# Kernel optimization log

Hardware: AMD Instinct MI355X
Metric: run time of the kernel (lower is better)

## Reference

```python
import jax, jax.numpy as jnp
import numpy as np

NUM_EXPERTS = 8
TOP_K = 2

def setup_inputs() -> dict:
    key = jax.random.key(0)
    k1, k2, k3, k4 = jax.random.split(key, 4)
    B, T, C, F = 4, 2048, 1024, 4096
    x = jax.random.normal(k1, (B, T, C), dtype=jnp.float32)
    gate_w = jax.random.normal(k2, (C, NUM_EXPERTS), dtype=jnp.float32) * 0.02
    w1 = jax.random.normal(k3, (NUM_EXPERTS, C, F), dtype=jnp.float32) * 0.02
    w2 = jax.random.normal(k4, (NUM_EXPERTS, F, C), dtype=jnp.float32) * 0.02
    return {"x": x, "gate_w": gate_w, "w1": w1, "w2": w2}

def reference(x, gate_w, w1, w2):
    # Router: softmax over experts, then top-k and renormalize
    router_logits = jnp.einsum('btc,ce->bte', x, gate_w)          # [B,T,E]
    routing = jax.nn.softmax(router_logits, axis=-1)
    topw, topi = jax.lax.top_k(routing, TOP_K)                    # [B,T,K]
    topw = topw / jnp.sum(topw, axis=-1, keepdims=True)
    # Combined per-expert weight per token (zero if not selected)
    onehot = jax.nn.one_hot(topi, NUM_EXPERTS, dtype=x.dtype)     # [B,T,K,E]
    combine = jnp.einsum('btk,btke->bte', topw, onehot)           # [B,T,E]
    # Expert FFNs (exact GELU, matching torch nn.GELU default)
    out = jnp.zeros_like(x)
    for e in range(NUM_EXPERTS):
        h = jax.nn.gelu(jnp.einsum('btc,cf->btf', x, w1[e]), approximate=False)
        y = jnp.einsum('btf,fc->btc', h, w2[e])
        out = out + combine[..., e:e+1] * y
    return out
```

## Files before the change

### kernel.cpp

```cpp
#include <hip/hip_runtime.h>
#include <hip/hip_bf16.h>
#include <math.h>

#define NUM_EXPERTS 8
#define NTOK 8192
#define CDIM 1024
#define FDIM 4096
#define MAXSLOTS 17408
#define MAXTILES 136
#define TILES_PER_XCD 17

typedef __bf16 bf16x8 __attribute__((ext_vector_type(8)));
typedef float  f32x4  __attribute__((ext_vector_type(4)));

#define GPTR(p) ((const __attribute__((address_space(1))) unsigned int*)(p))
#define LPTR(p) ((__attribute__((address_space(3))) unsigned int*)(p))

__device__ __forceinline__ float gelu_exact(float v){
  return 0.5f * v * (1.0f + erff(v * 0.70710678118654752f));
}
__device__ __forceinline__ float bf2f(unsigned short u){
  union { unsigned int i; float f; } cv; cv.i = ((unsigned int)u) << 16; return cv.f;
}

__global__ __launch_bounds__(256) void moe_router(
    const float* __restrict__ x, const float* __restrict__ gw,
    int2* __restrict__ topi, float2* __restrict__ topw, int* __restrict__ counts)
{
  int token = blockIdx.x * 4 + (threadIdx.x >> 6);
  int lane  = threadIdx.x & 63;
  int e = lane & 7, part = lane >> 3;
  const float* xr = x + (size_t)token * CDIM;
  float s = 0.f;
  int c0 = part * 128;
  for (int c = c0; c < c0 + 128; ++c) s += xr[c] * gw[c * 8 + e];
  s += __shfl_xor(s, 8); s += __shfl_xor(s, 16); s += __shfl_xor(s, 32);
  float m1 = s; int i1 = e;
  for (int off = 1; off < 8; off <<= 1){
    float ov = __shfl_xor(m1, off); int oi = __shfl_xor(i1, off);
    if (ov > m1 || (ov == m1 && oi < i1)){ m1 = ov; i1 = oi; }
  }
  float l2 = (e == i1) ? -INFINITY : s;
  float m2 = l2; int i2 = e;
  for (int off = 1; off < 8; off <<= 1){
    float ov = __shfl_xor(m2, off); int oi = __shfl_xor(i2, off);
    if (ov > m2 || (ov == m2 && oi < i2)){ m2 = ov; i2 = oi; }
  }
  if (lane == 0){
    float r = expf(m2 - m1);
    float wa = 1.f / (1.f + r);
    topi[token] = make_int2(i1, i2);
    topw[token] = make_float2(wa, 1.f - wa);
    atomicAdd(&counts[i1], 1);
    atomicAdd(&counts[i2], 1);
  }
}

__global__ __launch_bounds__(256) void convert_x_kernel(
    const float* __restrict__ x, __hip_bfloat16* __restrict__ xb)
{
  int i = (blockIdx.x * 256 + threadIdx.x) * 4;
  float4 v = *(const float4*)(x + i);
  union { __hip_bfloat16 hh[4]; ushort4 u; } cv;
  cv.hh[0] = __float2bfloat16(v.x);
  cv.hh[1] = __float2bfloat16(v.y);
  cv.hh[2] = __float2bfloat16(v.z);
  cv.hh[3] = __float2bfloat16(v.w);
  *(ushort4*)(xb + i) = cv.u;
}

__global__ __launch_bounds__(256) void transpose_bf16_kernel(
    const float* __restrict__ in, __hip_bfloat16* __restrict__ outp, int R, int Cc)
{
  __shared__ __hip_bfloat16 tile[64 * 66];
  const size_t msz = (size_t)R * Cc;
  const float* inm = in + (size_t)blockIdx.z * msz;
  __hip_bfloat16* outm = outp + (size_t)blockIdx.z * msz;
  int r0 = blockIdx.y * 64, c0 = blockIdx.x * 64;
  int t = threadIdx.x;
  int r = t & 63, cseg = (t >> 6) * 16;
  const float* src = inm + (size_t)(r0 + r) * Cc + c0 + cseg;
  float4 v0 = ((const float4*)src)[0];
  float4 v1 = ((const float4*)src)[1];
  float4 v2 = ((const float4*)src)[2];
  float4 v3 = ((const float4*)src)[3];
  float vv[16] = {v0.x,v0.y,v0.z,v0.w, v1.x,v1.y,v1.z,v1.w,
                  v2.x,v2.y,v2.z,v2.w, v3.x,v3.y,v3.z,v3.w};
#pragma unroll
  for (int k = 0; k < 16; ++k)
    tile[(cseg + k) * 66 + r] = __float2bfloat16(vv[k]);
  __syncthreads();
#pragma unroll
  for (int p = 0; p < 2; ++p){
    int cc = p * 32 + (t >> 3), ch = (t & 7) * 8;
    const unsigned short* rowp = (const unsigned short*)tile + cc * 66 + ch;
    unsigned int a = *(const unsigned int*)(rowp + 0);
    unsigned int b = *(const unsigned int*)(rowp + 2);
    unsigned int c = *(const unsigned int*)(rowp + 4);
    unsigned int d = *(const unsigned int*)(rowp + 6);
    *(uint4*)(outm + (size_t)(c0 + cc) * R + r0 + ch) = make_uint4(a, b, c, d);
  }
}

__global__ void scan_kernel(const int* __restrict__ counts, int* cursors, int* num_tiles,
    int* tile_expert, int* tile_slotbase, int* slot_token, float* slot_weight)
{
  int t = threadIdx.x;
  if (t == 0){
    int base = 0, T = 0;
    for (int e = 0; e < NUM_EXPERTS; ++e){
      cursors[e] = base;
      int nt = (counts[e] + 127) >> 7;
      for (int i = 0; i < nt; ++i){ tile_expert[T] = e; tile_slotbase[T] = base + i * 128; ++T; }
      base += nt << 7;
    }
    *num_tiles = T;
  }
  for (int i = t; i < MAXSLOTS; i += 256){ slot_token[i] = 0; slot_weight[i] = 0.f; }
}

__global__ void assign_kernel(const int2* __restrict__ topi, const float2* __restrict__ topw,
    int* cursors, int* slot_token, float* slot_weight, int2* __restrict__ token_slots)
{
  int token = blockIdx.x * 256 + threadIdx.x;
  int2 ii = topi[token];
  float2 ww = topw[token];
  int p0 = atomicAdd(&cursors[ii.x], 1);
  slot_token[p0] = token; slot_weight[p0] = ww.x;
  int p1 = atomicAdd(&cursors[ii.y], 1);
  slot_token[p1] = token; slot_weight[p1] = ww.y;
  token_slots[token] = make_int2(p0, p1);
}

template<int KD, int ND, bool G1>
__global__ __launch_bounds__(512, 4) void moe_gemm(
    const __hip_bfloat16* __restrict__ A, const __hip_bfloat16* __restrict__ Bw,
    __hip_bfloat16* __restrict__ Out,
    const int* __restrict__ num_tiles, const int* __restrict__ tile_expert,
    const int* __restrict__ tile_slotbase, const int* __restrict__ slot_token)
{
  constexpr int NT = KD / 32;
  constexpr int NBLK = ND / 256;
  __shared__ __align__(16) char smem[73728];
  const int L = blockIdx.x;
  const int xcd = L & 7;
  const int jdec = L >> 3;
  const int tl = jdec / NBLK;
  const int nb = jdec % NBLK;
  const int tm = xcd * TILES_PER_XCD + tl;
  if (tm >= *num_tiles) return;
  const int e = tile_expert[tm];
  const int sbase = tile_slotbase[tm];
  const int n0 = nb * 256;
  const int t = threadIdx.x;
  const int lane = t & 63, wid = t >> 6;
  const int wm = wid >> 2, wn = wid & 3;
  const int lr = lane & 15, lq = lane >> 4;

  const int arowi = sbase + wid * 16 + lr;
  const int arow = G1 ? slot_token[arowi] : arowi;
  const __hip_bfloat16* srcA  = A  + (size_t)arow * KD + lq * 8;
  const __hip_bfloat16* srcB0 = Bw + ((size_t)e * ND + n0 + wid * 16 + lr) * KD + lq * 8;
  const __hip_bfloat16* srcB1 = srcB0 + (size_t)128 * KD;
  char* dA  = smem + wid * 1024;
  char* dB0 = smem + 24576 + wid * 1024;
  char* dB1 = dB0 + 8192;

#define STG_A(kt, ss) __builtin_amdgcn_global_load_lds(GPTR(srcA + (size_t)(kt) * 32), LPTR(dA + (ss) * 8192), 16, 0, 0)
#define STG_B(kt, ss) do{ \
    __builtin_amdgcn_global_load_lds(GPTR(srcB0 + (size_t)(kt) * 32), LPTR(dB0 + (ss) * 16384), 16, 0, 0); \
    __builtin_amdgcn_global_load_lds(GPTR(srcB1 + (size_t)(kt) * 32), LPTR(dB1 + (ss) * 16384), 16, 0, 0); }while(0)

  STG_A(0, 0); STG_B(0, 0);
  STG_A(1, 1); STG_B(1, 1);

  f32x4 acc[4][4] = {};
  const char* rdA = smem + (wm * 4) * 1024 + lane * 16;
  const char* rdB = smem + 24576 + (wn * 4) * 1024 + lane * 16;

  asm volatile("s_waitcnt vmcnt(3)\n\ts_barrier" ::: "memory");
  __builtin_amdgcn_sched_barrier(0);

  int s = 0;
  for (int kt = 0; kt < NT; ++kt){
    int s2 = s + 2; if (s2 >= 3) s2 -= 3;
    const char* pA = rdA + s * 8192;
    const char* pB = rdB + s * 16384;
    bf16x8 b0 = *(const bf16x8*)(pB);
    bf16x8 b1 = *(const bf16x8*)(pB + 1024);
    bf16x8 b2 = *(const bf16x8*)(pB + 2048);
    bf16x8 b3 = *(const bf16x8*)(pB + 3072);
    bf16x8 a0 = *(const bf16x8*)(pA);
    bf16x8 a1 = *(const bf16x8*)(pA + 1024);
    if (kt + 2 < NT) STG_A(kt + 2, s2);
    __builtin_amdgcn_s_setprio(1);
    acc[0][0] = __builtin_amdgcn_mfma_f32_16x16x32_bf16(b0, a0, acc[0][0], 0, 0, 0);
    acc[0][1] = __builtin_amdgcn_mfma_f32_16x16x32_bf16(b1, a0, acc[0][1], 0, 0, 0);
    acc[0][2] = __builtin_amdgcn_mfma_f32_16x16x32_bf16(b2, a0, acc[0][2], 0, 0, 0);
    acc[0][3] = __builtin_amdgcn_mfma_f32_16x16x32_bf16(b3, a0, acc[0][3], 0, 0, 0);
    acc[1][0] = __builtin_amdgcn_mfma_f32_16x16x32_bf16(b0, a1, acc[1][0], 0, 0, 0);
    acc[1][1] = __builtin_amdgcn_mfma_f32_16x16x32_bf16(b1, a1, acc[1][1], 0, 0, 0);
    acc[1][2] = __builtin_amdgcn_mfma_f32_16x16x32_bf16(b2, a1, acc[1][2], 0, 0, 0);
    acc[1][3] = __builtin_amdgcn_mfma_f32_16x16x32_bf16(b3, a1, acc[1][3], 0, 0, 0);
    __builtin_amdgcn_s_setprio(0);
    a0 = *(const bf16x8*)(pA + 2048);
    a1 = *(const bf16x8*)(pA + 3072);
    if (kt + 2 < NT) STG_B(kt + 2, s2);
    __builtin_amdgcn_s_setprio(1);
    acc[2][0] = __builtin_amdgcn_mfma_f32_16x16x32_bf16(b0, a0, acc[2][0], 0, 0, 0);
    acc[2][1] = __builtin_amdgcn_mfma_f32_16x16x32_bf16(b1, a0, acc[2][1], 0, 0, 0);
    acc[2][2] = __builtin_amdgcn_mfma_f32_16x16x32_bf16(b2, a0, acc[2][2], 0, 0, 0);
    acc[2][3] = __builtin_amdgcn_mfma_f32_16x16x32_bf16(b3, a0, acc[2][3], 0, 0, 0);
    acc[3][0] = __builtin_amdgcn_mfma_f32_16x16x32_bf16(b0, a1, acc[3][0], 0, 0, 0);
    acc[3][1] = __builtin_amdgcn_mfma_f32_16x16x32_bf16(b1, a1, acc[3][1], 0, 0, 0);
    acc[3][2] = __builtin_amdgcn_mfma_f32_16x16x32_bf16(b2, a1, acc[3][2], 0, 0, 0);
    acc[3][3] = __builtin_amdgcn_mfma_f32_16x16x32_bf16(b3, a1, acc[3][3], 0, 0, 0);
    __builtin_amdgcn_s_setprio(0);
    if (kt < NT - 2){
      asm volatile("s_waitcnt vmcnt(3)\n\ts_barrier" ::: "memory");
      __builtin_amdgcn_sched_barrier(0);
    } else if (kt < NT - 1){
      asm volatile("s_waitcnt vmcnt(0)\n\ts_barrier" ::: "memory");
      __builtin_amdgcn_sched_barrier(0);
    }
    s = (s == 2) ? 0 : s + 1;
  }
#undef STG_A
#undef STG_B

  const int orow0 = sbase + wm * 64 + lr;
  const int ocol0 = n0 + wn * 64 + lq * 4;
#pragma unroll
  for (int i = 0; i < 4; ++i){
    __hip_bfloat16* orow = Out + (size_t)(orow0 + i * 16) * ND + ocol0;
#pragma unroll
    for (int j2 = 0; j2 < 4; ++j2){
      f32x4 v = acc[i][j2];
      union { __hip_bfloat16 h4[4]; ushort4 u; } cv;
      if (G1){
        cv.h4[0] = __float2bfloat16(gelu_exact(v[0]));
        cv.h4[1] = __float2bfloat16(gelu_exact(v[1]));
        cv.h4[2] = __float2bfloat16(gelu_exact(v[2]));
        cv.h4[3] = __float2bfloat16(gelu_exact(v[3]));
      } else {
        cv.h4[0] = __float2bfloat16(v[0]);
        cv.h4[1] = __float2bfloat16(v[1]);
        cv.h4[2] = __float2bfloat16(v[2]);
        cv.h4[3] = __float2bfloat16(v[3]);
      }
      *(ushort4*)(orow + j2 * 16) = cv.u;
    }
  }
}

__global__ __launch_bounds__(256) void combine_kernel(
    const __hip_bfloat16* __restrict__ y, const int2* __restrict__ token_slots,
    const float* __restrict__ slot_weight, float* __restrict__ out)
{
  int token = blockIdx.x;
  int c = threadIdx.x * 4;
  int2 ss = token_slots[token];
  float w0 = slot_weight[ss.x], w1 = slot_weight[ss.y];
  ushort4 a = *(const ushort4*)((const unsigned short*)y + (size_t)ss.x * CDIM + c);
  ushort4 b = *(const ushort4*)((const unsigned short*)y + (size_t)ss.y * CDIM + c);
  float4 o;
  o.x = w0 * bf2f(a.x) + w1 * bf2f(b.x);
  o.y = w0 * bf2f(a.y) + w1 * bf2f(b.y);
  o.z = w0 * bf2f(a.z) + w1 * bf2f(b.z);
  o.w = w0 * bf2f(a.w) + w1 * bf2f(b.w);
  *(float4*)(out + (size_t)token * CDIM + c) = o;
}

__global__ __launch_bounds__(256) void naive_kernel(
    const float* __restrict__ x, const float* __restrict__ w1, const float* __restrict__ w2,
    const int2* __restrict__ topi, const float2* __restrict__ topw, float* __restrict__ out)
{
  __shared__ float xs[CDIM];
  __shared__ float hs[FDIM];
  int token = blockIdx.x;
  int t = threadIdx.x;
  for (int i = t; i < CDIM; i += 256) xs[i] = x[(size_t)token * CDIM + i];
  float acc[4] = {0.f, 0.f, 0.f, 0.f};
  int2 ei = topi[token]; float2 ew = topw[token];
  int elist[2] = {ei.x, ei.y}; float wlist[2] = {ew.x, ew.y};
  for (int kk = 0; kk < 2; ++kk){
    int e = elist[kk]; float wgt = wlist[kk];
    __syncthreads();
    for (int f = t; f < FDIM; f += 256){
      const float* wcol = w1 + (size_t)e * CDIM * FDIM + f;
      float s = 0.f;
      for (int c = 0; c < CDIM; ++c) s += xs[c] * wcol[(size_t)c * FDIM];
      hs[f] = gelu_exact(s);
    }
    __syncthreads();
    for (int ii = 0; ii < 4; ++ii){
      int c = ii * 256 + t;
      const float* w2col = w2 + (size_t)e * FDIM * CDIM + c;
      float s = 0.f;
      for (int f = 0; f < FDIM; ++f) s += hs[f] * w2col[(size_t)f * CDIM];
      acc[ii] += wgt * s;
    }
  }
  for (int ii = 0; ii < 4; ++ii) out[(size_t)token * CDIM + ii * 256 + t] = acc[ii];
}

extern "C" void kernel_launch(void* const* d_in, const int* in_sizes, int n_in,
                              void* d_out, int out_size, void* d_ws, size_t ws_size,
                              hipStream_t stream)
{
  const float* x  = (const float*)d_in[0];
  const float* gw = (const float*)d_in[1];
  const float* w1 = (const float*)d_in[2];
  const float* w2 = (const float*)d_in[3];
  float* out = (float*)d_out;
  char* ws = (char*)d_ws;

  int*    counts        = (int*)(ws + 0);
  int*    cursors       = (int*)(ws + 32);
  int*    num_tiles     = (int*)(ws + 64);
  int*    tile_expert   = (int*)(ws + 256);
  int*    tile_slotbase = (int*)(ws + 1024);
  int2*   topi          = (int2*)(ws + 4096);
  float2* topw          = (float2*)(ws + 69632);
  int*    slot_token    = (int*)(ws + 135168);
  float*  slot_weight   = (float*)(ws + 204800);
  int2*   token_slots   = (int2*)(ws + 278528);
  const size_t XBF_OFF = 1u << 20;
  const size_t W1T_OFF = XBF_OFF + (size_t)NTOK * CDIM * 2;
  const size_t W2T_OFF = W1T_OFF + (size_t)NUM_EXPERTS * CDIM * FDIM * 2;
  const size_t H_OFF   = W2T_OFF + (size_t)NUM_EXPERTS * CDIM * FDIM * 2;
  const size_t NEED    = H_OFF + (size_t)MAXSLOTS * FDIM * 2;
  __hip_bfloat16* xbf = (__hip_bfloat16*)(ws + XBF_OFF);
  __hip_bfloat16* w1t = (__hip_bfloat16*)(ws + W1T_OFF);
  __hip_bfloat16* w2t = (__hip_bfloat16*)(ws + W2T_OFF);
  __hip_bfloat16* h   = (__hip_bfloat16*)(ws + H_OFF);
  __hip_bfloat16* y   = (__hip_bfloat16*)(ws + W1T_OFF);

  hipMemsetAsync(ws, 0, 4096, stream);

  moe_router<<<NTOK / 4, 256, 0, stream>>>(x, gw, topi, topw, counts);

  if (ws_size >= NEED){
    convert_x_kernel<<<NTOK * CDIM / (4 * 256), 256, 0, stream>>>(x, xbf);
    transpose_bf16_kernel<<<dim3(FDIM / 64, CDIM / 64, NUM_EXPERTS), 256, 0, stream>>>(w1, w1t, CDIM, FDIM);
    transpose_bf16_kernel<<<dim3(CDIM / 64, FDIM / 64, NUM_EXPERTS), 256, 0, stream>>>(w2, w2t, FDIM, CDIM);
    scan_kernel<<<1, 256, 0, stream>>>(counts, cursors, num_tiles, tile_expert, tile_slotbase, slot_token, slot_weight);
    assign_kernel<<<NTOK / 256, 256, 0, stream>>>(topi, topw, cursors, slot_token, slot_weight, token_slots);
    moe_gemm<CDIM, FDIM, true ><<<8 * TILES_PER_XCD * (FDIM / 256), 512, 0, stream>>>(
        xbf, w1t, h, num_tiles, tile_expert, tile_slotbase, slot_token);
    moe_gemm<FDIM, CDIM, false><<<8 * TILES_PER_XCD * (CDIM / 256), 512, 0, stream>>>(
        h, w2t, y, num_tiles, tile_expert, tile_slotbase, slot_token);
    combine_kernel<<<NTOK, 256, 0, stream>>>(y, token_slots, slot_weight, out);
  } else {
    naive_kernel<<<NTOK, 256, 0, stream>>>(x, w1, w2, topi, topw, out);
  }
}
```

Baseline: 1.132 ms.

## Double K-tile depth to 64 with XOR-swizzled LDS layout in MoE GEMM

New measurement: 995.0 us. -12.1%, faster.

```diff
diff --git a/kernel.cpp b/kernel.cpp
--- a/kernel.cpp
+++ b/kernel.cpp
@@ -133,15 +133,15 @@
 }
 
 template<int KD, int ND, bool G1>
-__global__ __launch_bounds__(512, 4) void moe_gemm(
+__global__ __launch_bounds__(512, 2) void moe_gemm(
     const __hip_bfloat16* __restrict__ A, const __hip_bfloat16* __restrict__ Bw,
     __hip_bfloat16* __restrict__ Out,
     const int* __restrict__ num_tiles, const int* __restrict__ tile_expert,
     const int* __restrict__ tile_slotbase, const int* __restrict__ slot_token)
 {
-  constexpr int NT = KD / 32;
+  constexpr int NT = KD / 64;
   constexpr int NBLK = ND / 256;
-  __shared__ __align__(16) char smem[73728];
+  __shared__ __align__(16) char smem[147456];
   const int L = blockIdx.x;
   const int xcd = L & 7;
   const int jdec = L >> 3;
@@ -157,42 +157,62 @@
   const int wm = wid >> 2, wn = wid & 3;
   const int lr = lane & 15, lq = lane >> 4;
 
-  const int arowi = sbase + wid * 16 + lr;
-  const int arow = G1 ? slot_token[arowi] : arowi;
-  const __hip_bfloat16* srcA  = A  + (size_t)arow * KD + lq * 8;
-  const __hip_bfloat16* srcB0 = Bw + ((size_t)e * ND + n0 + wid * 16 + lr) * KD + lq * 8;
-  const __hip_bfloat16* srcB1 = srcB0 + (size_t)128 * KD;
-  char* dA  = smem + wid * 1024;
-  char* dB0 = smem + 24576 + wid * 1024;
-  char* dB1 = dB0 + 8192;
-
-#define STG_A(kt, ss) __builtin_amdgcn_global_load_lds(GPTR(srcA + (size_t)(kt) * 32), LPTR(dA + (ss) * 8192), 16, 0, 0)
-#define STG_B(kt, ss) do{ \
-    __builtin_amdgcn_global_load_lds(GPTR(srcB0 + (size_t)(kt) * 32), LPTR(dB0 + (ss) * 16384), 16, 0, 0); \
-    __builtin_amdgcn_global_load_lds(GPTR(srcB1 + (size_t)(kt) * 32), LPTR(dB1 + (ss) * 16384), 16, 0, 0); }while(0)
-
-  STG_A(0, 0); STG_B(0, 0);
-  STG_A(1, 1); STG_B(1, 1);
+  const int srow = lane >> 3;
+  const int sch  = (lane & 7) ^ srow;
+  const __hip_bfloat16* sA[2];
+  const __hip_bfloat16* sB4[4];
+#pragma unroll
+  for (int hh = 0; hh < 2; ++hh){
+    int rA = (wid + 8 * hh) * 8 + srow;
+    int grow = G1 ? slot_token[sbase + rA] : (sbase + rA);
+    sA[hh] = A + (size_t)grow * KD + sch * 8;
+  }
+#pragma unroll
+  for (int hh = 0; hh < 4; ++hh){
+    int rB = (wid + 8 * hh) * 8 + srow;
+    sB4[hh] = Bw + ((size_t)e * ND + n0 + rB) * KD + sch * 8;
+  }
+  char* dA0 = smem + wid * 1024;
+  char* dB0 = smem + 49152 + wid * 1024;
+
+#define STAGE_A(ss) do{ \
+    __builtin_amdgcn_global_load_lds(GPTR(sA[0]), LPTR(dA0 + (ss) * 16384 + 0 * 8192), 16, 0, 0); \
+    __builtin_amdgcn_global_load_lds(GPTR(sA[1]), LPTR(dA0 + (ss) * 16384 + 1 * 8192), 16, 0, 0); }while(0)
+#define STAGE_B(ss) do{ \
+    __builtin_amdgcn_global_load_lds(GPTR(sB4[0]), LPTR(dB0 + (ss) * 32768 + 0 * 8192), 16, 0, 0); \
+    __builtin_amdgcn_global_load_lds(GPTR(sB4[1]), LPTR(dB0 + (ss) * 32768 + 1 * 8192), 16, 0, 0); \
+    __builtin_amdgcn_global_load_lds(GPTR(sB4[2]), LPTR(dB0 + (ss) * 32768 + 2 * 8192), 16, 0, 0); \
+    __builtin_amdgcn_global_load_lds(GPTR(sB4[3]), LPTR(dB0 + (ss) * 32768 + 3 * 8192), 16, 0, 0); }while(0)
+#define ADV() do{ sA[0]+=64; sA[1]+=64; sB4[0]+=64; sB4[1]+=64; sB4[2]+=64; sB4[3]+=64; }while(0)
+
+  STAGE_A(0); STAGE_B(0); ADV();
+  STAGE_A(1); STAGE_B(1); ADV();
 
   f32x4 acc[4][4] = {};
-  const char* rdA = smem + (wm * 4) * 1024 + lane * 16;
-  const char* rdB = smem + 24576 + (wn * 4) * 1024 + lane * 16;
-
-  asm volatile("s_waitcnt vmcnt(3)\n\ts_barrier" ::: "memory");
+  const char* rdA = smem + (wm * 64 + lr) * 128;
+  const char* rdB = smem + 49152 + (wn * 64 + lr) * 128;
+  const int x7 = lr & 7;
+  const int swz0 = ((0 | lq) ^ x7) * 16;
+  const int swz1 = ((4 | lq) ^ x7) * 16;
+
+  asm volatile("s_waitcnt vmcnt(6)\n\ts_barrier" ::: "memory");
   __builtin_amdgcn_sched_barrier(0);
 
   int s = 0;
   for (int kt = 0; kt < NT; ++kt){
     int s2 = s + 2; if (s2 >= 3) s2 -= 3;
-    const char* pA = rdA + s * 8192;
-    const char* pB = rdB + s * 16384;
-    bf16x8 b0 = *(const bf16x8*)(pB);
-    bf16x8 b1 = *(const bf16x8*)(pB + 1024);
-    bf16x8 b2 = *(const bf16x8*)(pB + 2048);
-    bf16x8 b3 = *(const bf16x8*)(pB + 3072);
-    bf16x8 a0 = *(const bf16x8*)(pA);
-    bf16x8 a1 = *(const bf16x8*)(pA + 1024);
-    if (kt + 2 < NT) STG_A(kt + 2, s2);
+    const char* pA = rdA + s * 16384;
+    const char* pB = rdB + s * 32768;
+    bf16x8 a0 = *(const bf16x8*)(pA + 0 * 2048 + swz0);
+    bf16x8 a1 = *(const bf16x8*)(pA + 1 * 2048 + swz0);
+    bf16x8 a2 = *(const bf16x8*)(pA + 2 * 2048 + swz0);
+    bf16x8 a3 = *(const bf16x8*)(pA + 3 * 2048 + swz0);
+    bf16x8 b0 = *(const bf16x8*)(pB + 0 * 2048 + swz0);
+    bf16x8 b1 = *(const bf16x8*)(pB + 1 * 2048 + swz0);
+    bf16x8 b2 = *(const bf16x8*)(pB + 2 * 2048 + swz0);
+    bf16x8 b3 = *(const bf16x8*)(pB + 3 * 2048 + swz0);
+    const bool pf = (kt + 2 < NT);
+    if (pf) STAGE_A(s2);
     __builtin_amdgcn_s_setprio(1);
     acc[0][0] = __builtin_amdgcn_mfma_f32_16x16x32_bf16(b0, a0, acc[0][0], 0, 0, 0);
     acc[0][1] = __builtin_amdgcn_mfma_f32_16x16x32_bf16(b1, a0, acc[0][1], 0, 0, 0);
@@ -202,22 +222,44 @@
     acc[1][1] = __builtin_amdgcn_mfma_f32_16x16x32_bf16(b1, a1, acc[1][1], 0, 0, 0);
     acc[1][2] = __builtin_amdgcn_mfma_f32_16x16x32_bf16(b2, a1, acc[1][2], 0, 0, 0);
     acc[1][3] = __builtin_amdgcn_mfma_f32_16x16x32_bf16(b3, a1, acc[1][3], 0, 0, 0);
+    acc[2][0] = __builtin_amdgcn_mfma_f32_16x16x32_bf16(b0, a2, acc[2][0], 0, 0, 0);
+    acc[2][1] = __builtin_amdgcn_mfma_f32_16x16x32_bf16(b1, a2, acc[2][1], 0, 0, 0);
+    acc[2][2] = __builtin_amdgcn_mfma_f32_16x16x32_bf16(b2, a2, acc[2][2], 0, 0, 0);
+    acc[2][3] = __builtin_amdgcn_mfma_f32_16x16x32_bf16(b3, a2, acc[2][3], 0, 0, 0);
+    acc[3][0] = __builtin_amdgcn_mfma_f32_16x16x32_bf16(b0, a3, acc[3][0], 0, 0, 0);
+    acc[3][1] = __builtin_amdgcn_mfma_f32_16x16x32_bf16(b1, a3, acc[3][1], 0, 0, 0);
+    acc[3][2] = __builtin_amdgcn_mfma_f32_16x16x32_bf16(b2, a3, acc[3][2], 0, 0, 0);
+    acc[3][3] = __builtin_amdgcn_mfma_f32_16x16x32_bf16(b3, a3, acc[3][3], 0, 0, 0);
     __builtin_amdgcn_s_setprio(0);
-    a0 = *(const bf16x8*)(pA + 2048);
-    a1 = *(const bf16x8*)(pA + 3072);
-    if (kt + 2 < NT) STG_B(kt + 2, s2);
+    a0 = *(const bf16x8*)(pA + 0 * 2048 + swz1);
+    a1 = *(const bf16x8*)(pA + 1 * 2048 + swz1);
+    a2 = *(const bf16x8*)(pA + 2 * 2048 + swz1);
+    a3 = *(const bf16x8*)(pA + 3 * 2048 + swz1);
+    b0 = *(const bf16x8*)(pB + 0 * 2048 + swz1);
+    b1 = *(const bf16x8*)(pB + 1 * 2048 + swz1);
+    b2 = *(const bf16x8*)(pB + 2 * 2048 + swz1);
+    b3 = *(const bf16x8*)(pB + 3 * 2048 + swz1);
+    if (pf){ STAGE_B(s2); ADV(); }
     __builtin_amdgcn_s_setprio(1);
-    acc[2][0] = __builtin_amdgcn_mfma_f32_16x16x32_bf16(b0, a0, acc[2][0], 0, 0, 0);
-    acc[2][1] = __builtin_amdgcn_mfma_f32_16x16x32_bf16(b1, a0, acc[2][1], 0, 0, 0);
-    acc[2][2] = __builtin_amdgcn_mfma_f32_16x16x32_bf16(b2, a0, acc[2][2], 0, 0, 0);
-    acc[2][3] = __builtin_amdgcn_mfma_f32_16x16x32_bf16(b3, a0, acc[2][3], 0, 0, 0);
-    acc[3][0] = __builtin_amdgcn_mfma_f32_16x16x32_bf16(b0, a1, acc[3][0], 0, 0, 0);
-    acc[3][1] = __builtin_amdgcn_mfma_f32_16x16x32_bf16(b1, a1, acc[3][1], 0, 0, 0);
-    acc[3][2] = __builtin_amdgcn_mfma_f32_16x16x32_bf16(b2, a1, acc[3][2], 0, 0, 0);
-    acc[3][3] = __builtin_amdgcn_mfma_f32_16x16x32_bf16(b3, a1, acc[3][3], 0, 0, 0);
+    acc[0][0] = __builtin_amdgcn_mfma_f32_16x16x32_bf16(b0, a0, acc[0][0], 0, 0, 0);
+    acc[0][1] = __builtin_amdgcn_mfma_f32_16x16x32_bf16(b1, a0, acc[0][1], 0, 0, 0);
+    acc[0][2] = __builtin_amdgcn_mfma_f32_16x16x32_bf16(b2, a0, acc[0][2], 0, 0, 0);
+    acc[0][3] = __builtin_amdgcn_mfma_f32_16x16x32_bf16(b3, a0, acc[0][3], 0, 0, 0);
+    acc[1][0] = __builtin_amdgcn_mfma_f32_16x16x32_bf16(b0, a1, acc[1][0], 0, 0, 0);
+    acc[1][1] = __builtin_amdgcn_mfma_f32_16x16x32_bf16(b1, a1, acc[1][1], 0, 0, 0);
+    acc[1][2] = __builtin_amdgcn_mfma_f32_16x16x32_bf16(b2, a1, acc[1][2], 0, 0, 0);
+    acc[1][3] = __builtin_amdgcn_mfma_f32_16x16x32_bf16(b3, a1, acc[1][3], 0, 0, 0);
+    acc[2][0] = __builtin_amdgcn_mfma_f32_16x16x32_bf16(b0, a2, acc[2][0], 0, 0, 0);
+    acc[2][1] = __builtin_amdgcn_mfma_f32_16x16x32_bf16(b1, a2, acc[2][1], 0, 0, 0);
+    acc[2][2] = __builtin_amdgcn_mfma_f32_16x16x32_bf16(b2, a2, acc[2][2], 0, 0, 0);
+    acc[2][3] = __builtin_amdgcn_mfma_f32_16x16x32_bf16(b3, a2, acc[2][3], 0, 0, 0);
+    acc[3][0] = __builtin_amdgcn_mfma_f32_16x16x32_bf16(b0, a3, acc[3][0], 0, 0, 0);
+    acc[3][1] = __builtin_amdgcn_mfma_f32_16x16x32_bf16(b1, a3, acc[3][1], 0, 0, 0);
+    acc[3][2] = __builtin_amdgcn_mfma_f32_16x16x32_bf16(b2, a3, acc[3][2], 0, 0, 0);
+    acc[3][3] = __builtin_amdgcn_mfma_f32_16x16x32_bf16(b3, a3, acc[3][3], 0, 0, 0);
     __builtin_amdgcn_s_setprio(0);
     if (kt < NT - 2){
-      asm volatile("s_waitcnt vmcnt(3)\n\ts_barrier" ::: "memory");
+      asm volatile("s_waitcnt vmcnt(6)\n\ts_barrier" ::: "memory");
       __builtin_amdgcn_sched_barrier(0);
     } else if (kt < NT - 1){
       asm volatile("s_waitcnt vmcnt(0)\n\ts_barrier" ::: "memory");
@@ -225,8 +267,9 @@
     }
     s = (s == 2) ? 0 : s + 1;
   }
-#undef STG_A
-#undef STG_B
+#undef STAGE_A
+#undef STAGE_B
+#undef ADV
 
   const int orow0 = sbase + wm * 64 + lr;
   const int ocol0 = n0 + wn * 64 + lq * 4;
```

## Enlarge MoE GEMM tiles to 256x256 with K=64 steps and swizzled LDS

Applied to the files above, without the earlier changes.

Result: faster. 1.026 ms (-9.3%).

```diff
diff --git a/kernel.cpp b/kernel.cpp
--- a/kernel.cpp
+++ b/kernel.cpp
@@ -6,15 +6,16 @@
 #define NTOK 8192
 #define CDIM 1024
 #define FDIM 4096
-#define MAXSLOTS 17408
-#define MAXTILES 136
-#define TILES_PER_XCD 17
+#define MAXSLOTS 18432
+#define MAXTILES 72
+#define TILES_PER_XCD 9
 
 typedef __bf16 bf16x8 __attribute__((ext_vector_type(8)));
 typedef float  f32x4  __attribute__((ext_vector_type(4)));
 
 #define GPTR(p) ((const __attribute__((address_space(1))) unsigned int*)(p))
 #define LPTR(p) ((__attribute__((address_space(3))) unsigned int*)(p))
+#define MFMA16(b, a, c) __builtin_amdgcn_mfma_f32_16x16x32_bf16((b), (a), (c), 0, 0, 0)
 
 __device__ __forceinline__ float gelu_exact(float v){
   return 0.5f * v * (1.0f + erff(v * 0.70710678118654752f));
@@ -110,9 +111,9 @@
     int base = 0, T = 0;
     for (int e = 0; e < NUM_EXPERTS; ++e){
       cursors[e] = base;
-      int nt = (counts[e] + 127) >> 7;
-      for (int i = 0; i < nt; ++i){ tile_expert[T] = e; tile_slotbase[T] = base + i * 128; ++T; }
-      base += nt << 7;
+      int nt = (counts[e] + 255) >> 8;
+      for (int i = 0; i < nt; ++i){ tile_expert[T] = e; tile_slotbase[T] = base + i * 256; ++T; }
+      base += nt << 8;
     }
     *num_tiles = T;
   }
@@ -133,15 +134,15 @@
 }
 
 template<int KD, int ND, bool G1>
-__global__ __launch_bounds__(512, 4) void moe_gemm(
+__global__ __launch_bounds__(512, 2) void moe_gemm(
     const __hip_bfloat16* __restrict__ A, const __hip_bfloat16* __restrict__ Bw,
     __hip_bfloat16* __restrict__ Out,
     const int* __restrict__ num_tiles, const int* __restrict__ tile_expert,
     const int* __restrict__ tile_slotbase, const int* __restrict__ slot_token)
 {
-  constexpr int NT = KD / 32;
+  constexpr int NT = KD / 64;
   constexpr int NBLK = ND / 256;
-  __shared__ __align__(16) char smem[73728];
+  __shared__ __align__(16) char smem[131072];
   const int L = blockIdx.x;
   const int xcd = L & 7;
   const int jdec = L >> 3;
@@ -157,85 +158,92 @@
   const int wm = wid >> 2, wn = wid & 3;
   const int lr = lane & 15, lq = lane >> 4;
 
-  const int arowi = sbase + wid * 16 + lr;
-  const int arow = G1 ? slot_token[arowi] : arowi;
-  const __hip_bfloat16* srcA  = A  + (size_t)arow * KD + lq * 8;
-  const __hip_bfloat16* srcB0 = Bw + ((size_t)e * ND + n0 + wid * 16 + lr) * KD + lq * 8;
-  const __hip_bfloat16* srcB1 = srcB0 + (size_t)128 * KD;
-  char* dA  = smem + wid * 1024;
-  char* dB0 = smem + 24576 + wid * 1024;
-  char* dB1 = dB0 + 8192;
-
-#define STG_A(kt, ss) __builtin_amdgcn_global_load_lds(GPTR(srcA + (size_t)(kt) * 32), LPTR(dA + (ss) * 8192), 16, 0, 0)
-#define STG_B(kt, ss) do{ \
-    __builtin_amdgcn_global_load_lds(GPTR(srcB0 + (size_t)(kt) * 32), LPTR(dB0 + (ss) * 16384), 16, 0, 0); \
-    __builtin_amdgcn_global_load_lds(GPTR(srcB1 + (size_t)(kt) * 32), LPTR(dB1 + (ss) * 16384), 16, 0, 0); }while(0)
-
-  STG_A(0, 0); STG_B(0, 0);
-  STG_A(1, 1); STG_B(1, 1);
-
-  f32x4 acc[4][4] = {};
-  const char* rdA = smem + (wm * 4) * 1024 + lane * 16;
-  const char* rdB = smem + 24576 + (wn * 4) * 1024 + lane * 16;
-
-  asm volatile("s_waitcnt vmcnt(3)\n\ts_barrier" ::: "memory");
-  __builtin_amdgcn_sched_barrier(0);
-
-  int s = 0;
+  const int lr6 = t >> 3;
+  const int sub = lr6 >> 5, rr = lr6 & 31;
+  const int sch = (t & 7) ^ (rr & 7);
+  const __hip_bfloat16* sA[4];
+  const __hip_bfloat16* sB[4];
+#pragma unroll
+  for (int g = 0; g < 4; ++g){
+    int trow = sub * 128 + g * 32 + rr;
+    int ar = G1 ? slot_token[sbase + trow] : (sbase + trow);
+    sA[g] = A + (size_t)ar * KD + sch * 8;
+    sB[g] = Bw + ((size_t)e * ND + n0 + trow) * KD + sch * 8;
+  }
+  char* dA = smem + wid * 1024;
+  char* dB = smem + 65536 + wid * 1024;
+
+#define STG(gg, ktt) do{ const int par_ = (ktt) & 1; \
+    __builtin_amdgcn_global_load_lds(GPTR(sA[gg] + (size_t)(ktt) * 64), LPTR(dA + par_ * 32768 + (gg) * 8192), 16, 0, 0); \
+    __builtin_amdgcn_global_load_lds(GPTR(sB[gg] + (size_t)(ktt) * 64), LPTR(dB + par_ * 32768 + (gg) * 8192), 16, 0, 0); }while(0)
+
+  int offA[8], offB[4];
+#pragma unroll
+  for (int f = 0; f < 8; ++f)
+    offA[f] = ((f >> 1) * 64 + wm * 32 + (f & 1) * 16 + lr) * 128;
+#pragma unroll
+  for (int j = 0; j < 4; ++j)
+    offB[j] = (((wn & 1) * 2 + (j >> 1)) * 64 + (wn >> 1) * 32 + (j & 1) * 16 + lr) * 128;
+  const int swz0 = ((0 + lq) ^ (lr & 7)) * 16;
+  const int swz1 = ((4 + lq) ^ (lr & 7)) * 16;
+
+  STG(0, 0); STG(1, 0); STG(2, 0); STG(3, 0);
+  STG(0, 1); STG(1, 1); STG(2, 1); STG(3, 1);
+  f32x4 acc[8][4] = {};
+  asm volatile("s_waitcnt vmcnt(8)" ::: "memory");
+  __builtin_amdgcn_s_barrier();
+
+  bf16x8 bB[4][2];
   for (int kt = 0; kt < NT; ++kt){
-    int s2 = s + 2; if (s2 >= 3) s2 -= 3;
-    const char* pA = rdA + s * 8192;
-    const char* pB = rdB + s * 16384;
-    bf16x8 b0 = *(const bf16x8*)(pB);
-    bf16x8 b1 = *(const bf16x8*)(pB + 1024);
-    bf16x8 b2 = *(const bf16x8*)(pB + 2048);
-    bf16x8 b3 = *(const bf16x8*)(pB + 3072);
-    bf16x8 a0 = *(const bf16x8*)(pA);
-    bf16x8 a1 = *(const bf16x8*)(pA + 1024);
-    if (kt + 2 < NT) STG_A(kt + 2, s2);
-    __builtin_amdgcn_s_setprio(1);
-    acc[0][0] = __builtin_amdgcn_mfma_f32_16x16x32_bf16(b0, a0, acc[0][0], 0, 0, 0);
-    acc[0][1] = __builtin_amdgcn_mfma_f32_16x16x32_bf16(b1, a0, acc[0][1], 0, 0, 0);
-    acc[0][2] = __builtin_amdgcn_mfma_f32_16x16x32_bf16(b2, a0, acc[0][2], 0, 0, 0);
-    acc[0][3] = __builtin_amdgcn_mfma_f32_16x16x32_bf16(b3, a0, acc[0][3], 0, 0, 0);
-    acc[1][0] = __builtin_amdgcn_mfma_f32_16x16x32_bf16(b0, a1, acc[1][0], 0, 0, 0);
-    acc[1][1] = __builtin_amdgcn_mfma_f32_16x16x32_bf16(b1, a1, acc[1][1], 0, 0, 0);
-    acc[1][2] = __builtin_amdgcn_mfma_f32_16x16x32_bf16(b2, a1, acc[1][2], 0, 0, 0);
-    acc[1][3] = __builtin_amdgcn_mfma_f32_16x16x32_bf16(b3, a1, acc[1][3], 0, 0, 0);
-    __builtin_amdgcn_s_setprio(0);
-    a0 = *(const bf16x8*)(pA + 2048);
-    a1 = *(const bf16x8*)(pA + 3072);
-    if (kt + 2 < NT) STG_B(kt + 2, s2);
-    __builtin_amdgcn_s_setprio(1);
-    acc[2][0] = __builtin_amdgcn_mfma_f32_16x16x32_bf16(b0, a0, acc[2][0], 0, 0, 0);
-    acc[2][1] = __builtin_amdgcn_mfma_f32_16x16x32_bf16(b1, a0, acc[2][1], 0, 0, 0);
-    acc[2][2] = __builtin_amdgcn_mfma_f32_16x16x32_bf16(b2, a0, acc[2][2], 0, 0, 0);
-    acc[2][3] = __builtin_amdgcn_mfma_f32_16x16x32_bf16(b3, a0, acc[2][3], 0, 0, 0);
-    acc[3][0] = __builtin_amdgcn_mfma_f32_16x16x32_bf16(b0, a1, acc[3][0], 0, 0, 0);
-    acc[3][1] = __builtin_amdgcn_mfma_f32_16x16x32_bf16(b1, a1, acc[3][1], 0, 0, 0);
-    acc[3][2] = __builtin_amdgcn_mfma_f32_16x16x32_bf16(b2, a1, acc[3][2], 0, 0, 0);
-    acc[3][3] = __builtin_amdgcn_mfma_f32_16x16x32_bf16(b3, a1, acc[3][3], 0, 0, 0);
-    __builtin_amdgcn_s_setprio(0);
-    if (kt < NT - 2){
-      asm volatile("s_waitcnt vmcnt(3)\n\ts_barrier" ::: "memory");
-      __builtin_amdgcn_sched_barrier(0);
-    } else if (kt < NT - 1){
-      asm volatile("s_waitcnt vmcnt(0)\n\ts_barrier" ::: "memory");
-      __builtin_amdgcn_sched_barrier(0);
-    }
-    s = (s == 2) ? 0 : s + 1;
-  }
-#undef STG_A
-#undef STG_B
-
-  const int orow0 = sbase + wm * 64 + lr;
+    const int par = kt & 1;
+    const char* pA = smem + par * 32768;
+    const char* pB = smem + 65536 + par * 32768;
+#pragma unroll
+    for (int q = 0; q < 4; ++q){
+      if (q == 0){
+#pragma unroll
+        for (int j = 0; j < 4; ++j){
+          bB[j][0] = *(const bf16x8*)(pB + offB[j] + swz0);
+          bB[j][1] = *(const bf16x8*)(pB + offB[j] + swz1);
+        }
+      }
+      bf16x8 a00 = *(const bf16x8*)(pA + offA[2*q]     + swz0);
+      bf16x8 a01 = *(const bf16x8*)(pA + offA[2*q]     + swz1);
+      bf16x8 a10 = *(const bf16x8*)(pA + offA[2*q + 1] + swz0);
+      bf16x8 a11 = *(const bf16x8*)(pA + offA[2*q + 1] + swz1);
+      const int ktt = (q == 0) ? (kt + 1) : (kt + 2);
+      const int gg = (q + 3) & 3;
+      if (ktt >= 2 && ktt < NT) STG(gg, ktt);
+      __builtin_amdgcn_s_barrier();
+      __builtin_amdgcn_s_setprio(1);
+#pragma unroll
+      for (int j = 0; j < 4; ++j){
+        acc[2*q][j]     = MFMA16(bB[j][0], a00, acc[2*q][j]);
+        acc[2*q + 1][j] = MFMA16(bB[j][0], a10, acc[2*q + 1][j]);
+      }
+#pragma unroll
+      for (int j = 0; j < 4; ++j){
+        acc[2*q][j]     = MFMA16(bB[j][1], a01, acc[2*q][j]);
+        acc[2*q + 1][j] = MFMA16(bB[j][1], a11, acc[2*q + 1][j]);
+      }
+      __builtin_amdgcn_s_setprio(0);
+      if (q == 3){
+        if (kt < NT - 2) asm volatile("s_waitcnt vmcnt(6)" ::: "memory");
+        else             asm volatile("s_waitcnt vmcnt(0)" ::: "memory");
+      }
+      if (!(kt == NT - 1 && q == 3)) __builtin_amdgcn_s_barrier();
+    }
+  }
+#undef STG
+
+  const int orow0 = sbase + wm * 128 + lr;
   const int ocol0 = n0 + wn * 64 + lq * 4;
 #pragma unroll
-  for (int i = 0; i < 4; ++i){
-    __hip_bfloat16* orow = Out + (size_t)(orow0 + i * 16) * ND + ocol0;
-#pragma unroll
-    for (int j2 = 0; j2 < 4; ++j2){
-      f32x4 v = acc[i][j2];
+  for (int f = 0; f < 8; ++f){
+    __hip_bfloat16* orow = Out + (size_t)(orow0 + f * 16) * ND + ocol0;
+#pragma unroll
+    for (int j = 0; j < 4; ++j){
+      f32x4 v = acc[f][j];
       union { __hip_bfloat16 h4[4]; ushort4 u; } cv;
       if (G1){
         cv.h4[0] = __float2bfloat16(gelu_exact(v[0]));
@@ -248,7 +256,7 @@
         cv.h4[2] = __float2bfloat16(v[2]);
         cv.h4[3] = __float2bfloat16(v[3]);
       }
-      *(ushort4*)(orow + j2 * 16) = cv.u;
+      *(ushort4*)(orow + j * 16) = cv.u;
     }
   }
 }
@@ -323,8 +331,8 @@
   int2*   topi          = (int2*)(ws + 4096);
   float2* topw          = (float2*)(ws + 69632);
   int*    slot_token    = (int*)(ws + 135168);
-  float*  slot_weight   = (float*)(ws + 204800);
-  int2*   token_slots   = (int2*)(ws + 278528);
+  float*  slot_weight   = (float*)(ws + 208896);
+  int2*   token_slots   = (int2*)(ws + 282624);
   const size_t XBF_OFF = 1u << 20;
   const size_t W1T_OFF = XBF_OFF + (size_t)NTOK * CDIM * 2;
   const size_t W2T_OFF = W1T_OFF + (size_t)NUM_EXPERTS * CDIM * FDIM * 2;
```
